# Optimization experiments

Measured on AMD Instinct MI355X. Metric: run time of the kernel, lower is better.

Reference implementation:

```python
import jax, jax.numpy as jnp
import numpy as np

N, F, E = 50000, 128, 800000
U0, H0, A0 = 64, 8, 8
U1, H1, A1 = 40, 1, 1


def setup_inputs() -> dict:
    key = jax.random.key(0)
    ks = jax.random.split(key, 10)
    s = lambda fan: 1.0 / np.sqrt(fan)
    return {
        "x": jax.random.normal(ks[0], (N, F), jnp.float32),
        "edge_index": jax.random.randint(ks[1], (2, E), 0, N, jnp.int32),
        "wq0": jax.random.normal(ks[2], (F, H0 * A0), jnp.float32) * s(F),
        "bq0": jnp.zeros((H0 * A0,), jnp.float32),
        "wk0": jax.random.normal(ks[3], (F, H0 * A0), jnp.float32) * s(F),
        "bk0": jnp.zeros((H0 * A0,), jnp.float32),
        "wv0": jax.random.normal(ks[4], (F, U0), jnp.float32) * s(F),
        "b0": jnp.zeros((U0,), jnp.float32),
        "wq1": jax.random.normal(ks[5], (U0, H1 * A1), jnp.float32) * s(U0),
        "bq1": jnp.zeros((H1 * A1,), jnp.float32),
        "wk1": jax.random.normal(ks[6], (U0, H1 * A1), jnp.float32) * s(U0),
        "bk1": jnp.zeros((H1 * A1,), jnp.float32),
        "wv1": jax.random.normal(ks[7], (U0, U1), jnp.float32) * s(U0),
        "b1": jnp.zeros((U1,), jnp.float32),
    }


def _gat_layer(x, row, col, wq, bq, wk, bk, wv, b, num_heads, activation):
    # tf_geometric GAT: relu(Q), relu(K), per-head dot-product attention with
    # segment softmax over destination node (row), scatter-weighted sum of V.
    n = x.shape[0]
    a_units = wq.shape[1] // num_heads
    d_head = wv.shape[1] // num_heads
    Q = jax.nn.relu(x @ wq + bq).reshape(n, num_heads, a_units)[row]   # [E,H,A]
    K = jax.nn.relu(x @ wk + bk).reshape(n, num_heads, a_units)[col]   # [E,H,A]
    att = jnp.sum(Q * K, axis=-1) / jnp.sqrt(jnp.float32(a_units))     # [E,H]
    m = jax.lax.stop_gradient(jax.ops.segment_max(att, row, num_segments=n))
    e = jnp.exp(att - m[row])
    denom = jax.ops.segment_sum(e, row, num_segments=n)                # [N,H]
    alpha = e / denom[row]                                             # [E,H]
    V = (x @ wv).reshape(n, num_heads, d_head)[col]                    # [E,H,D]
    out = jax.ops.segment_sum(V * alpha[..., None], row, num_segments=n)
    out = out.reshape(n, num_heads * d_head) + b
    return activation(out)


def reference(x, edge_index, wq0, bq0, wk0, bk0, wv0, b0,
              wq1, bq1, wk1, bk1, wv1, b1):
    n = x.shape[0]
    loops = jnp.arange(n, dtype=edge_index.dtype)
    ei = jnp.concatenate([edge_index, jnp.stack([loops, loops])], axis=1)
    row, col = ei[0], ei[1]
    h = _gat_layer(x, row, col, wq0, bq0, wk0, bk0, wv0, b0, H0, jax.nn.relu)
    h = _gat_layer(h, row, col, wq1, bq1, wk1, bk1, wv1, b1, H1, lambda v: v)
    return h
```

## Files before the change

kernel.cpp:

```cpp
#include <hip/hip_runtime.h>
#include <hip/hip_bf16.h>
#include <math.h>

#define Fdim 128
#define CAP 32
#define SM_SHIFT 20.0f

typedef __attribute__((ext_vector_type(8))) short bf16x8;
typedef __attribute__((ext_vector_type(4))) float f32x4;

__device__ __forceinline__ unsigned short f2bf(float x) {
    __hip_bfloat16 h = __float2bfloat16(x);
    return *(unsigned short*)&h;
}
__device__ __forceinline__ unsigned int pk2bf(float a, float b) {
    return (unsigned int)f2bf(a) | ((unsigned int)f2bf(b) << 16);
}
__device__ __forceinline__ float bflo(unsigned int u) {
    unsigned int b = u << 16;
    return *(float*)&b;
}
__device__ __forceinline__ float bfhi(unsigned int u) {
    unsigned int b = u & 0xffff0000u;
    return *(float*)&b;
}

__global__ void k_wt(const float* __restrict__ wq, const float* __restrict__ wk,
                     const float* __restrict__ wv, unsigned short* __restrict__ WT) {
    int t = blockIdx.x * blockDim.x + threadIdx.x;
    if (t >= 192 * Fdim) return;
    int c = t >> 7, k = t & 127;
    float v = (c < 64) ? wq[k * 64 + c]
            : (c < 128) ? wk[k * 64 + (c - 64)]
                        : wv[k * 64 + (c - 128)];
    WT[t] = f2bf(v);
}

__global__ __launch_bounds__(256) void k_node0adj(
    const float* __restrict__ x,
    const unsigned short* __restrict__ WT,
    const float* __restrict__ bq, const float* __restrict__ bk,
    float* __restrict__ Q0, unsigned int* __restrict__ KV0,
    const int* __restrict__ row, const int* __restrict__ col,
    int* __restrict__ cnt, unsigned short* __restrict__ adj,
    unsigned int* __restrict__ spill, int* __restrict__ spill_cnt,
    int E_, int Etot, int n) {
    int t = threadIdx.x;
    {
        int p = blockIdx.x & 7;
        int gb = blockIdx.x >> 3;
        int ngb = gridDim.x >> 3;
        if (gb < ngb) {
            int quarter = (Etot + 3) >> 2;
            int stride = ngb * 256;
            for (int base = gb * 256 + t; base < quarter; base += stride) {
                #pragma unroll
                for (int qd = 0; qd < 4; ++qd) {
                    int e = base + qd * quarter;
                    if (e < Etot) {
                        int r, c;
                        if (e < E_) { r = row[e]; c = col[e]; } else { r = e - E_; c = r; }
                        if (((r >> 4) & 7) == p) {
                            int pos = atomicAdd(&cnt[r], 1);
                            if (pos < CAP) {
                                adj[(size_t)r * CAP + pos] = (unsigned short)c;
                            } else {
                                int sp = atomicAdd(spill_cnt, 1);
                                spill[sp] = ((unsigned int)r << 16) | (unsigned int)c;
                            }
                        }
                    }
                }
            }
        }
    }
    int wv_ = t >> 6;
    int ln = t & 63;
    int rowbase = blockIdx.x * 64 + wv_ * 16;
    if (rowbase >= n) return;
    int cl = ln & 15;
    int kgrp = (ln >> 4) * 8;
    int arow = rowbase + cl;
    int arowc = min(arow, n - 1);
    f32x4 acc[12];
    #pragma unroll
    for (int i = 0; i < 12; ++i) acc[i] = (f32x4)(0.f);
    #pragma unroll
    for (int ks = 0; ks < 4; ++ks) {
        int k0 = ks * 32 + kgrp;
        const float4* xp = (const float4*)(x + (size_t)arowc * Fdim + k0);
        float4 xa = xp[0], xb = xp[1];
        union { unsigned int u[4]; bf16x8 v; } af;
        af.u[0] = pk2bf(xa.x, xa.y);
        af.u[1] = pk2bf(xa.z, xa.w);
        af.u[2] = pk2bf(xb.x, xb.y);
        af.u[3] = pk2bf(xb.z, xb.w);
        #pragma unroll
        for (int tt = 0; tt < 12; ++tt) {
            bf16x8 bf = *(const bf16x8*)(WT + (size_t)(tt * 16 + cl) * Fdim + k0);
            acc[tt] = __builtin_amdgcn_mfma_f32_16x16x32_bf16(af.v, bf, acc[tt], 0, 0, 0);
        }
    }
    int rgrp = (ln >> 4) * 4;
    #pragma unroll
    for (int r = 0; r < 4; ++r) {
        int node = rowbase + rgrp + r;
        if (node < n) {
            #pragma unroll
            for (int tq = 0; tq < 4; ++tq) {
                float q = fmaxf(acc[tq][r] + bq[tq * 16 + cl], 0.f);
                Q0[(size_t)node * 64 + tq * 16 + cl] = q;
            }
            #pragma unroll
            for (int tk = 0; tk < 4; ++tk) {
                float kk = fmaxf(acc[4 + tk][r] + bk[tk * 16 + cl], 0.f);
                float vv = acc[8 + tk][r];
                KV0[(size_t)node * 64 + tk * 16 + cl] =
                    (unsigned int)f2bf(kk) | ((unsigned int)f2bf(vv) << 16);
            }
        }
    }
}

__global__ void k_spill0(const int* __restrict__ spill_cnt,
                         const unsigned int* __restrict__ spill,
                         const float* __restrict__ Q0,
                         const unsigned int* __restrict__ KV0,
                         float* __restrict__ extra0) {
    int sc = *spill_cnt;
    int widx = (blockIdx.x * blockDim.x + threadIdx.x) >> 6;
    int nw = (gridDim.x * blockDim.x) >> 6;
    int j = threadIdx.x & 63;
    for (int i = widx; i < sc; i += nw) {
        unsigned int pc = spill[i];
        int r = pc >> 16, c = pc & 0xFFFF;
        float q = Q0[(size_t)r * 64 + j] * 0.35355339059327373f;
        unsigned int kv = KV0[(size_t)c * 64 + j];
        float p = q * bflo(kv);
        #pragma unroll
        for (int off = 1; off < 8; off <<= 1) p += __shfl_xor(p, off);
        float w = __expf(p - SM_SHIFT);
        atomicAdd(&extra0[(size_t)r * 72 + 8 + j], w * bfhi(kv));
        if ((j & 7) == 0) atomicAdd(&extra0[(size_t)r * 72 + (j >> 3)], w);
    }
}

__global__ void k_spill1(const int* __restrict__ spill_cnt,
                         const unsigned int* __restrict__ spill,
                         const float* __restrict__ Q1, const float* __restrict__ K1,
                         const unsigned short* __restrict__ V1u,
                         float* __restrict__ extra1) {
    int sc = *spill_cnt;
    int widx = (blockIdx.x * blockDim.x + threadIdx.x) >> 6;
    int nw = (gridDim.x * blockDim.x) >> 6;
    int j = threadIdx.x & 63;
    for (int i = widx; i < sc; i += nw) {
        unsigned int pc = spill[i];
        int r = pc >> 16, c = pc & 0xFFFF;
        float w = __expf(Q1[r] * K1[c] - SM_SHIFT);
        if (j < 40) {
            float v = bflo((unsigned int)V1u[(size_t)c * 40 + j]);
            atomicAdd(&extra1[(size_t)r * 44 + 4 + j], w * v);
        } else if (j == 63) {
            atomicAdd(&extra1[(size_t)r * 44], w);
        }
    }
}

__global__ __launch_bounds__(256) void k_fuse0(
    const int* __restrict__ cnt, const unsigned short* __restrict__ adj,
    const float* __restrict__ Q0, const unsigned int* __restrict__ KV0,
    const float* __restrict__ extra0, const int* __restrict__ spillc,
    const float* __restrict__ b0,
    const float* __restrict__ wq1, const float* __restrict__ bq1,
    const float* __restrict__ wk1, const float* __restrict__ bk1,
    const float* __restrict__ wv1,
    float* __restrict__ Q1, float* __restrict__ K1,
    unsigned short* __restrict__ V1u, int n) {
    __shared__ float hs[8][64];
    int wid = threadIdx.x >> 6;
    int lane = threadIdx.x & 63;
    int sub = lane >> 5;
    int l = lane & 31;
    int half = wid * 2 + sub;
    int node = blockIdx.x * 8 + half;
    if (node >= n) return;
    const float SC = 0.35355339059327373f;
    float2 qp = ((const float2*)(Q0 + (size_t)node * 64))[l];
    float q0 = qp.x * SC, q1 = qp.y * SC;
    int end = min(cnt[node], CAP);
    int myadj = (int)adj[(size_t)node * CAP + l];
    int sbase = sub * 32;
    float s[4]  = {0.f, 0.f, 0.f, 0.f};
    float aA[4] = {0.f, 0.f, 0.f, 0.f};
    float aB[4] = {0.f, 0.f, 0.f, 0.f};
    if (*spillc != 0) {
        s[0] = extra0[(size_t)node * 72 + (l >> 2)];
        float2 ea = ((const float2*)(extra0 + (size_t)node * 72 + 8))[l];
        aA[0] = ea.x; aB[0] = ea.y;
    }
    for (int e = 0; e < end; e += 16) {
        int m = end - e;
        int c[16];
        #pragma unroll
        for (int i = 0; i < 16; ++i)
            c[i] = __shfl(myadj, sbase + min(e + i, end - 1));
        uint2 kv[16];
        #pragma unroll
        for (int i = 0; i < 16; ++i)
            kv[i] = ((const uint2*)(KV0 + (size_t)c[i] * 64))[l];
        float p[16];
        #pragma unroll
        for (int i = 0; i < 16; ++i)
            p[i] = q0 * bflo(kv[i].x) + q1 * bflo(kv[i].y);
        #pragma unroll
        for (int off = 1; off < 4; off <<= 1) {
            #pragma unroll
            for (int i = 0; i < 16; ++i)
                p[i] += __shfl_xor(p[i], off);
        }
        #pragma unroll
        for (int i = 0; i < 16; ++i) {
            float w = (i == 0 || m > i) ? __expf(p[i] - SM_SHIFT) : 0.f;
            s[i & 3]  += w;
            aA[i & 3] += w * bfhi(kv[i].x);
            aB[i & 3] += w * bfhi(kv[i].y);
        }
    }
    float ssum = (s[0] + s[1]) + (s[2] + s[3]);
    float aAs  = (aA[0] + aA[1]) + (aA[2] + aA[3]);
    float aBs  = (aB[0] + aB[1]) + (aB[2] + aB[3]);
    float2 bp = ((const float2*)b0)[l];
    float h0 = fmaxf(aAs / ssum + bp.x, 0.f);
    float h1 = fmaxf(aBs / ssum + bp.y, 0.f);
    ((float2*)hs[half])[l] = make_float2(h0, h1);
    {
        int colB = 32 + l;
        const float* wA = wv1 + l;
        const float* wB = (colB < 40) ? (wv1 + colB)
                        : ((colB == 40) ? wq1 : wk1);
        int strideB = (colB < 40) ? 40 : 1;
        float accA = 0.f, accB = 0.f;
        #pragma unroll 4
        for (int k = 0; k < 64; ++k) {
            float hk = hs[half][k];
            accA += hk * wA[k * 40];
            accB += hk * wB[k * strideB];
        }
        V1u[(size_t)node * 40 + l] = f2bf(accA);
        if (colB < 40) {
            V1u[(size_t)node * 40 + colB] = f2bf(accB);
        } else if (colB == 40) {
            Q1[node] = fmaxf(accB + bq1[0], 0.f);
        } else if (colB == 41) {
            K1[node] = fmaxf(accB + bk1[0], 0.f);
        }
    }
}

__global__ __launch_bounds__(256) void k_fuse1(
    const int* __restrict__ cnt, const unsigned short* __restrict__ adj,
    const float* __restrict__ Q1, const float* __restrict__ K1,
    const unsigned int* __restrict__ V1p, const float* __restrict__ extra1,
    const int* __restrict__ spillc, const float* __restrict__ b1,
    float* __restrict__ out, int n) {
    int wid = threadIdx.x >> 6;
    int lane = threadIdx.x & 63;
    int sub = lane >> 5;
    int l = lane & 31;
    int node = blockIdx.x * 8 + wid * 2 + sub;
    if (node >= n) return;
    float qr = Q1[node];
    int end = min(cnt[node], CAP);
    int myadj = (int)adj[(size_t)node * CAP + l];
    float wl = (l < end) ? __expf(qr * K1[myadj] - SM_SHIFT) : 0.f;
    float ssum = wl;
    #pragma unroll
    for (int off = 1; off < 32; off <<= 1) ssum += __shfl_xor(ssum, off);
    bool act = (l < 20);
    float aL[4] = {0.f, 0.f, 0.f, 0.f};
    float aH[4] = {0.f, 0.f, 0.f, 0.f};
    if (*spillc != 0) {
        ssum += extra1[(size_t)node * 44];
        if (act) {
            aL[0] = extra1[(size_t)node * 44 + 4 + 2 * l];
            aH[0] = extra1[(size_t)node * 44 + 5 + 2 * l];
        }
    }
    int sbase = sub * 32;
    for (int e = 0; e < end; e += 8) {
        float ww[8];
        int cc[8];
        #pragma unroll
        for (int i = 0; i < 8; ++i) {
            ww[i] = __shfl(wl, sbase + min(e + i, 31));
            cc[i] = __shfl(myadj, sbase + min(e + i, end - 1));
        }
        unsigned int pv[8];
        #pragma unroll
        for (int i = 0; i < 8; ++i)
            pv[i] = act ? V1p[(size_t)cc[i] * 20 + l] : 0u;
        #pragma unroll
        for (int i = 0; i < 8; ++i) {
            aL[i & 3] += ww[i] * bflo(pv[i]);
            aH[i & 3] += ww[i] * bfhi(pv[i]);
        }
    }
    float aLs = (aL[0] + aL[1]) + (aL[2] + aL[3]);
    float aHs = (aH[0] + aH[1]) + (aH[2] + aH[3]);
    if (act) {
        const float2* b1p = (const float2*)b1;
        float2 bb = b1p[l];
        float2 o;
        o.x = aLs / ssum + bb.x;
        o.y = aHs / ssum + bb.y;
        ((float2*)out)[(size_t)node * 20 + l] = o;
    }
}

extern "C" void kernel_launch(void* const* d_in, const int* in_sizes, int n_in,
                              void* d_out, int out_size, void* d_ws, size_t ws_size,
                              hipStream_t stream) {
    const float* x   = (const float*)d_in[0];
    const int*   ei  = (const int*)d_in[1];
    const float* wq0 = (const float*)d_in[2];
    const float* bq0 = (const float*)d_in[3];
    const float* wk0 = (const float*)d_in[4];
    const float* bk0 = (const float*)d_in[5];
    const float* wv0 = (const float*)d_in[6];
    const float* b0  = (const float*)d_in[7];
    const float* wq1 = (const float*)d_in[8];
    const float* bq1 = (const float*)d_in[9];
    const float* wk1 = (const float*)d_in[10];
    const float* bk1 = (const float*)d_in[11];
    const float* wv1 = (const float*)d_in[12];
    const float* b1  = (const float*)d_in[13];
    float* out = (float*)d_out;

    int n    = in_sizes[0] / Fdim;
    int E_   = in_sizes[1] / 2;
    int Etot = E_ + n;
    const int* row = ei;
    const int* col = ei + E_;

    float* ws = (float*)d_ws;
    float*          Q0     = ws;                   ws += (size_t)n * 64;
    unsigned int*   KV0    = (unsigned int*)ws;    ws += (size_t)n * 64;
    unsigned short* V1u    = (unsigned short*)ws;  ws += (size_t)n * 20;
    float*          Q1     = ws;                   ws += n;
    float*          K1     = ws;                   ws += n;
    unsigned short* adj    = (unsigned short*)ws;  ws += (size_t)n * (CAP / 2);
    unsigned short* WT     = (unsigned short*)ws;  ws += (192 * Fdim) / 2;
    int*            cnt    = (int*)ws;             ws += n;
    int*            spillc = (int*)ws;             ws += 4;
    float*          extra0 = ws;                   ws += (size_t)n * 72;
    float*          extra1 = ws;                   ws += (size_t)n * 44;
    unsigned int*   spill  = (unsigned int*)ws;

    size_t zero_bytes = ((size_t)n + 4 + (size_t)n * 72 + (size_t)n * 44) * 4;
    int ngrid0 = (n + 63) / 64;

    hipMemsetAsync(cnt, 0, zero_bytes, stream);
    k_wt<<<(192 * Fdim + 255) / 256, 256, 0, stream>>>(wq0, wk0, wv0, WT);

    k_node0adj<<<ngrid0, 256, 0, stream>>>(x, WT, bq0, bk0, Q0, KV0,
                                           row, col, cnt, adj,
                                           spill, spillc, E_, Etot, n);
    k_spill0<<<64, 256, 0, stream>>>(spillc, spill, Q0, KV0, extra0);

    k_fuse0<<<(n + 7) / 8, 256, 0, stream>>>(cnt, adj, Q0, KV0, extra0, spillc, b0,
                                             wq1, bq1, wk1, bk1, wv1,
                                             Q1, K1, V1u, n);
    k_spill1<<<64, 256, 0, stream>>>(spillc, spill, Q1, K1, V1u, extra1);

    k_fuse1<<<(n + 7) / 8, 256, 0, stream>>>(cnt, adj, Q1, K1,
                                             (const unsigned int*)V1u, extra1,
                                             spillc, b1, out, n);
}
```

Baseline: 184.6 us.

## Vectorize layer-0 edge gather to 16-byte loads and fold buffer zeroing into kernel

The layer-0 aggregation kernel now splits each 32-lane half-wave into two 16-lane groups. Each group handles a different edge and loads 16 bytes of packed K/V per lane instead of 8. This cuts the shuffle-reduction steps per edge and raises the bytes per memory transaction. The groups' partial sums are merged with a final xor shuffle. Separately, zeroing of the spill-correction buffers moves from a large memset into a grid-stride loop inside the node/adjacency kernel, which now launches a fixed 2048 blocks. This trades a separate fill pass for extra stores in that kernel, and it relies on the kernel tolerating the new grid size.

New measurement: 166.8 us. -9.6%, faster.

```diff
diff --git a/kernel.cpp b/kernel.cpp
--- a/kernel.cpp
+++ b/kernel.cpp
@@ -44,8 +44,15 @@
     const int* __restrict__ row, const int* __restrict__ col,
     int* __restrict__ cnt, unsigned short* __restrict__ adj,
     unsigned int* __restrict__ spill, int* __restrict__ spill_cnt,
+    float4* __restrict__ extra_zero, int extra_zero_q,
     int E_, int Etot, int n) {
     int t = threadIdx.x;
+    {
+        int stride = gridDim.x * 256;
+        float4 z = make_float4(0.f, 0.f, 0.f, 0.f);
+        for (int i = blockIdx.x * 256 + t; i < extra_zero_q; i += stride)
+            extra_zero[i] = z;
+    }
     {
         int p = blockIdx.x & 7;
         int gb = blockIdx.x >> 3;
@@ -182,58 +189,59 @@
     int lane = threadIdx.x & 63;
     int sub = lane >> 5;
     int l = lane & 31;
+    int sl = l >> 4;
+    int dl = l & 15;
     int half = wid * 2 + sub;
     int node = blockIdx.x * 8 + half;
     if (node >= n) return;
     const float SC = 0.35355339059327373f;
-    float2 qp = ((const float2*)(Q0 + (size_t)node * 64))[l];
-    float q0 = qp.x * SC, q1 = qp.y * SC;
+    float4 q4 = ((const float4*)(Q0 + (size_t)node * 64))[dl];
+    q4.x *= SC; q4.y *= SC; q4.z *= SC; q4.w *= SC;
     int end = min(cnt[node], CAP);
     int myadj = (int)adj[(size_t)node * CAP + l];
     int sbase = sub * 32;
-    float s[4]  = {0.f, 0.f, 0.f, 0.f};
-    float aA[4] = {0.f, 0.f, 0.f, 0.f};
-    float aB[4] = {0.f, 0.f, 0.f, 0.f};
-    if (*spillc != 0) {
-        s[0] = extra0[(size_t)node * 72 + (l >> 2)];
-        float2 ea = ((const float2*)(extra0 + (size_t)node * 72 + 8))[l];
-        aA[0] = ea.x; aB[0] = ea.y;
-    }
-    for (int e = 0; e < end; e += 16) {
-        int m = end - e;
-        int c[16];
-        #pragma unroll
-        for (int i = 0; i < 16; ++i)
-            c[i] = __shfl(myadj, sbase + min(e + i, end - 1));
-        uint2 kv[16];
-        #pragma unroll
-        for (int i = 0; i < 16; ++i)
-            kv[i] = ((const uint2*)(KV0 + (size_t)c[i] * 64))[l];
-        float p[16];
-        #pragma unroll
-        for (int i = 0; i < 16; ++i)
-            p[i] = q0 * bflo(kv[i].x) + q1 * bflo(kv[i].y);
-        #pragma unroll
-        for (int off = 1; off < 4; off <<= 1) {
-            #pragma unroll
-            for (int i = 0; i < 16; ++i)
-                p[i] += __shfl_xor(p[i], off);
-        }
-        #pragma unroll
-        for (int i = 0; i < 16; ++i) {
-            float w = (i == 0 || m > i) ? __expf(p[i] - SM_SHIFT) : 0.f;
-            s[i & 3]  += w;
-            aA[i & 3] += w * bfhi(kv[i].x);
-            aB[i & 3] += w * bfhi(kv[i].y);
-        }
-    }
-    float ssum = (s[0] + s[1]) + (s[2] + s[3]);
-    float aAs  = (aA[0] + aA[1]) + (aA[2] + aA[3]);
-    float aBs  = (aB[0] + aB[1]) + (aB[2] + aB[3]);
-    float2 bp = ((const float2*)b0)[l];
-    float h0 = fmaxf(aAs / ssum + bp.x, 0.f);
-    float h1 = fmaxf(aBs / ssum + bp.y, 0.f);
-    ((float2*)hs[half])[l] = make_float2(h0, h1);
+    float s = 0.f;
+    float accx = 0.f, accy = 0.f, accz = 0.f, accw = 0.f;
+    if (*spillc != 0 && sl == 0) {
+        s = extra0[(size_t)node * 72 + (dl >> 1)];
+        float4 ea = ((const float4*)(extra0 + (size_t)node * 72 + 8))[dl];
+        accx = ea.x; accy = ea.y; accz = ea.z; accw = ea.w;
+    }
+    for (int e = 0; e < end; e += 8) {
+        uint4 kv[4];
+        int idx[4];
+        #pragma unroll
+        for (int j = 0; j < 4; ++j) {
+            idx[j] = e + 2 * j + sl;
+            int c = __shfl(myadj, sbase + min(idx[j], end - 1));
+            kv[j] = ((const uint4*)(KV0 + (size_t)c * 64))[dl];
+        }
+        #pragma unroll
+        for (int j = 0; j < 4; ++j) {
+            float p = q4.x * bflo(kv[j].x) + q4.y * bflo(kv[j].y)
+                    + q4.z * bflo(kv[j].z) + q4.w * bflo(kv[j].w);
+            p += __shfl_xor(p, 1);
+            bool valid = (idx[j] == 0) | (idx[j] < end);
+            float w = valid ? __expf(p - SM_SHIFT) : 0.f;
+            s += w;
+            accx += w * bfhi(kv[j].x);
+            accy += w * bfhi(kv[j].y);
+            accz += w * bfhi(kv[j].z);
+            accw += w * bfhi(kv[j].w);
+        }
+    }
+    s    += __shfl_xor(s, 16);
+    accx += __shfl_xor(accx, 16);
+    accy += __shfl_xor(accy, 16);
+    accz += __shfl_xor(accz, 16);
+    accw += __shfl_xor(accw, 16);
+    float4 bp = ((const float4*)b0)[dl];
+    float4 h;
+    h.x = fmaxf(accx / s + bp.x, 0.f);
+    h.y = fmaxf(accy / s + bp.y, 0.f);
+    h.z = fmaxf(accz / s + bp.z, 0.f);
+    h.w = fmaxf(accw / s + bp.w, 0.f);
+    if (sl == 0) ((float4*)hs[half])[dl] = h;
     {
         int colB = 32 + l;
         const float* wA = wv1 + l;
@@ -357,15 +365,17 @@
     float*          extra1 = ws;                   ws += (size_t)n * 44;
     unsigned int*   spill  = (unsigned int*)ws;
 
-    size_t zero_bytes = ((size_t)n + 4 + (size_t)n * 72 + (size_t)n * 44) * 4;
-    int ngrid0 = (n + 63) / 64;
-
-    hipMemsetAsync(cnt, 0, zero_bytes, stream);
+    int extra_zero_q = (int)(((size_t)n * 72 + (size_t)n * 44) / 4);
+    int ngrid0 = 2048;
+
+    hipMemsetAsync(cnt, 0, ((size_t)n + 4) * sizeof(int), stream);
     k_wt<<<(192 * Fdim + 255) / 256, 256, 0, stream>>>(wq0, wk0, wv0, WT);
 
     k_node0adj<<<ngrid0, 256, 0, stream>>>(x, WT, bq0, bk0, Q0, KV0,
                                            row, col, cnt, adj,
-                                           spill, spillc, E_, Etot, n);
+                                           spill, spillc,
+                                           (float4*)extra0, extra_zero_q,
+                                           E_, Etot, n);
     k_spill0<<<64, 256, 0, stream>>>(spillc, spill, Q0, KV0, extra0);
 
     k_fuse0<<<(n + 7) / 8, 256, 0, stream>>>(cnt, adj, Q0, KV0, extra0, spillc, b0,
```
